# Performance work log

Measured on AMD Instinct MI355X. Metric: run time of the kernel, lower is better.

## Reference

```python
import jax, jax.numpy as jnp
import numpy as np

B, S, D, H = 2, 2048, 512, 8
DK = D // H


def setup_inputs() -> dict:
    key = jax.random.key(0)
    ks = jax.random.split(key, 7)
    scale = 1.0 / np.sqrt(D)
    return {
        "query": jax.random.normal(ks[0], (B, S, D), dtype=jnp.float32),
        "key": jax.random.normal(ks[1], (B, S, D), dtype=jnp.float32),
        "value": jax.random.normal(ks[2], (B, S, D), dtype=jnp.float32),
        "w_q": jax.random.normal(ks[3], (D, D), dtype=jnp.float32) * scale,
        "w_k": jax.random.normal(ks[4], (D, D), dtype=jnp.float32) * scale,
        "w_v": jax.random.normal(ks[5], (D, D), dtype=jnp.float32) * scale,
        "w_o": jax.random.normal(ks[6], (D, D), dtype=jnp.float32) * scale,
    }


def reference(query, key, value, w_q, w_k, w_v, w_o):
    # Linear projections (torch nn.Linear: x @ W.T), split into heads -> [b, h, s, dk]
    def proj(x, w):
        return (x @ w.T).reshape(B, -1, H, DK).transpose(0, 2, 1, 3)

    q = proj(query, w_q)
    k = proj(key, w_k)
    v = proj(value, w_v)

    # scaled dot-product attention (unfused, materializes [b,h,s,s] scores)
    scores = jnp.einsum("bhqd,bhkd->bhqk", q, k) / np.sqrt(DK)
    p_attn = jax.nn.softmax(scores, axis=-1)
    out = jnp.einsum("bhqk,bhkd->bhqd", p_attn, v)  # [b,h,s,dk]

    # merge heads and final projection
    out = out.transpose(0, 2, 1, 3).reshape(B, -1, D)
    out = out @ w_o.T
    return (out, p_attn)
```

## Files before the change

### kernel.cpp

```cpp
#include <hip/hip_runtime.h>
#include <hip/hip_bf16.h>
#include <cstdint>
#include <cstddef>

#define BB 2
#define SS 2048
#define DD 512
#define HH 8
#define DKK 64

typedef __attribute__((ext_vector_type(8))) short bf16x8;
typedef __attribute__((ext_vector_type(4))) float f32x4;

__device__ __forceinline__ unsigned short f2bf(float f) {
    union { float f; unsigned u; } v; v.f = f;
    unsigned u = v.u;
    return (unsigned short)((u + 0x7fffu + ((u >> 16) & 1u)) >> 16);
}
__device__ __forceinline__ unsigned pack2(float a, float b) {
    return (unsigned)f2bf(a) | ((unsigned)f2bf(b) << 16);
}

typedef const __attribute__((address_space(1))) unsigned int* gp_t;
typedef __attribute__((address_space(3))) unsigned int* lp_t;
__device__ __forceinline__ void gload_lds16(const void* g, void* l) {
    __builtin_amdgcn_global_load_lds((gp_t)g, (lp_t)l, 16, 0, 0);
}

#define VM_WAIT4 asm volatile("s_waitcnt vmcnt(4)" ::: "memory")
#define VM_WAIT0 asm volatile("s_waitcnt vmcnt(0)" ::: "memory")

template <bool ABF>
__device__ __forceinline__ void gemm64_core2(
    const void* __restrict__ Av, const float* __restrict__ W,
    unsigned short* smem, int bm, int bn, int tid, f32x4 acc[4])
{
    const int w = tid >> 6, lane = tid & 63, quad = lane >> 4, l15 = lane & 15;

    float4 ra[2][2], rw[2][2];
    auto loadRegs = [&](int k0) {
        if (!ABF) {
            const float* A = (const float*)Av;
            #pragma unroll
            for (int r = 0; r < 2; ++r) {
                int flat = r * 256 + tid;
                int row = flat >> 3, c = flat & 7, cs = c ^ (row & 7);
                const float* p = A + (size_t)(bm * 64 + row) * DD + k0 + cs * 8;
                ra[r][0] = *(const float4*)p;
                ra[r][1] = *(const float4*)(p + 4);
            }
        }
        #pragma unroll
        for (int r = 0; r < 2; ++r) {
            int flat = r * 256 + tid;
            int row = flat >> 3, c = flat & 7, cs = c ^ (row & 7);
            const float* p = W + (size_t)(bn * 64 + row) * DD + k0 + cs * 8;
            rw[r][0] = *(const float4*)p;
            rw[r][1] = *(const float4*)(p + 4);
        }
    };
    auto writeLDS = [&]() {
        #pragma unroll
        for (int r = 0; r < 2; ++r) {
            int flat = r * 256 + tid;
            if (!ABF)
                *(uint4*)&smem[flat * 8] = make_uint4(
                    pack2(ra[r][0].x, ra[r][0].y), pack2(ra[r][0].z, ra[r][0].w),
                    pack2(ra[r][1].x, ra[r][1].y), pack2(ra[r][1].z, ra[r][1].w));
            *(uint4*)&smem[4096 + flat * 8] = make_uint4(
                pack2(rw[r][0].x, rw[r][0].y), pack2(rw[r][0].z, rw[r][0].w),
                pack2(rw[r][1].x, rw[r][1].y), pack2(rw[r][1].z, rw[r][1].w));
        }
    };

    loadRegs(0);
    for (int k0 = 0; k0 < DD; k0 += 64) {
        if (ABF) {
            const unsigned short* A = (const unsigned short*)Av;
            #pragma unroll
            for (int r = 0; r < 2; ++r) {
                int flat = r * 256 + tid;
                int row = flat >> 3, c = flat & 7, cs = c ^ (row & 7);
                gload_lds16(A + (size_t)(bm * 64 + row) * DD + k0 + cs * 8, &smem[flat * 8]);
            }
        }
        writeLDS();
        __syncthreads();
        if (k0 + 64 < DD) loadRegs(k0 + 64);
        int mrow = w * 16 + l15;
        bf16x8 a0 = *(const bf16x8*)&smem[(mrow * 8 + (quad ^ (mrow & 7))) * 8];
        bf16x8 a1 = *(const bf16x8*)&smem[(mrow * 8 + ((quad + 4) ^ (mrow & 7))) * 8];
        #pragma unroll
        for (int nt = 0; nt < 4; ++nt) {
            int nrow = nt * 16 + l15;
            bf16x8 b0 = *(const bf16x8*)&smem[4096 + (nrow * 8 + (quad ^ (nrow & 7))) * 8];
            bf16x8 b1 = *(const bf16x8*)&smem[4096 + (nrow * 8 + ((quad + 4) ^ (nrow & 7))) * 8];
            acc[nt] = __builtin_amdgcn_mfma_f32_16x16x32_bf16(a0, b0, acc[nt], 0, 0, 0);
            acc[nt] = __builtin_amdgcn_mfma_f32_16x16x32_bf16(a1, b1, acc[nt], 0, 0, 0);
        }
        __syncthreads();
    }
}

__global__ __launch_bounds__(256) void k_gemm_qkv(
    const float* __restrict__ xq, const float* __restrict__ xk, const float* __restrict__ xv,
    const float* __restrict__ wq, const float* __restrict__ wk, const float* __restrict__ wv,
    unsigned short* __restrict__ Qw, unsigned short* __restrict__ Kw,
    unsigned short* __restrict__ Vt)
{
    __shared__ unsigned short smem[8192];
    const int z = blockIdx.z;
    const float* A = (z == 0) ? xq : (z == 1) ? xk : xv;
    const float* W = (z == 0) ? wq : (z == 1) ? wk : wv;
    const int bm = blockIdx.x, bn = blockIdx.y;
    const int tid = threadIdx.x, w = tid >> 6, lane = tid & 63, quad = lane >> 4, l15 = lane & 15;

    f32x4 acc[4];
    #pragma unroll
    for (int i = 0; i < 4; ++i) acc[i] = (f32x4){0.f, 0.f, 0.f, 0.f};
    gemm64_core2<false>(A, W, smem, bm, bn, tid, acc);

    if (z != 2) {
        const float sc = (z == 0) ? 0.125f : 1.0f;
        unsigned short* dbf = (z == 0) ? Qw : Kw;
        #pragma unroll
        for (int nt = 0; nt < 4; ++nt) {
            int n = bn * 64 + nt * 16 + l15;
            int h = n >> 6, dk = n & 63;
            #pragma unroll
            for (int rg = 0; rg < 4; ++rg) {
                int m = bm * 64 + w * 16 + quad * 4 + rg;
                int b = m >> 11, s = m & (SS - 1);
                dbf[(((size_t)(b * HH + h) * SS + s) << 6) + dk] = f2bf(acc[nt][rg] * sc);
            }
        }
    } else {
        unsigned short* T = smem;
        #pragma unroll
        for (int nt = 0; nt < 4; ++nt)
            #pragma unroll
            for (int rg = 0; rg < 4; ++rg)
                T[(w * 16 + quad * 4 + rg) * 72 + nt * 16 + l15] = f2bf(acc[nt][rg]);
        __syncthreads();
        int n = tid >> 2, s0 = (tid & 3) * 16;
        int ng = bn * 64 + n, h = ng >> 6, dk = ng & 63;
        int mg = bm * 64 + s0, b = mg >> 11, s = mg & (SS - 1);
        unsigned vals[8];
        #pragma unroll
        for (int i = 0; i < 8; ++i)
            vals[i] = (unsigned)T[(s0 + 2*i) * 72 + n] | ((unsigned)T[(s0 + 2*i + 1) * 72 + n] << 16);
        unsigned short* dp = Vt + ((size_t)(b * HH + h) * DKK + dk) * SS + s;
        ((uint4*)dp)[0] = make_uint4(vals[0], vals[1], vals[2], vals[3]);
        ((uint4*)dp)[1] = make_uint4(vals[4], vals[5], vals[6], vals[7]);
    }
}

__global__ __launch_bounds__(256) void k_attn(
    const unsigned short* __restrict__ Qw, const unsigned short* __restrict__ Kw,
    const unsigned short* __restrict__ Vt, unsigned short* __restrict__ AO,
    float* __restrict__ Linv)
{
    __shared__ unsigned short Kl[2][4096];
    __shared__ unsigned short Vl[2][4096];
    __shared__ unsigned short Pl[2][4][16][68];

    const int id = blockIdx.x;
    const int xcd = id & 7, j = id >> 3;
    const int bh = xcd * 2 + (j >> 5), qt = j & 31;

    const int tid = threadIdx.x, w = tid >> 6, lane = tid & 63, quad = lane >> 4, l15 = lane & 15;

    const unsigned short* Qb = Qw + ((size_t)bh * SS + qt * 64 + w * 16) * DKK;
    const unsigned short* Kb = Kw + (size_t)bh * SS * DKK;
    const unsigned short* Vb = Vt + (size_t)bh * DKK * SS;

    bf16x8 qa0 = *(const bf16x8*)&Qb[l15 * DKK + quad * 8];
    bf16x8 qa1 = *(const bf16x8*)&Qb[l15 * DKK + 32 + quad * 8];

    f32x4 oacc[4];
    #pragma unroll
    for (int i = 0; i < 4; ++i) oacc[i] = (f32x4){0.f, 0.f, 0.f, 0.f};
    float lsum[4] = {0.f, 0.f, 0.f, 0.f};

    auto stage = [&](int kt, int b) {
        #pragma unroll
        for (int r = 0; r < 2; ++r) {
            int flat = r * 256 + tid;
            int row = flat >> 3, c = flat & 7, cs = c ^ (row & 7);
            gload_lds16(Kb + (size_t)(kt * 64 + row) * DKK + cs * 8, &Kl[b][flat * 8]);
        }
        #pragma unroll
        for (int r = 0; r < 2; ++r) {
            int flat = r * 256 + tid;
            int row = flat >> 3, c = flat & 7, cs = c ^ (row & 7);
            gload_lds16(Vb + (size_t)row * SS + kt * 64 + cs * 8, &Vl[b][flat * 8]);
        }
    };

    stage(0, 0);
    stage(1, 1);

    const int NT = SS / 64;
    for (int kt = 0; kt < NT; ++kt) {
        if (kt < NT - 1) { VM_WAIT4; } else { VM_WAIT0; }
        __builtin_amdgcn_s_barrier();
        __builtin_amdgcn_sched_barrier(0);
        const int b = kt & 1;

        f32x4 sa[4];
        #pragma unroll
        for (int i = 0; i < 4; ++i) sa[i] = (f32x4){0.f, 0.f, 0.f, 0.f};
        __builtin_amdgcn_s_setprio(1);
        #pragma unroll
        for (int jt = 0; jt < 4; ++jt) {
            int row = jt * 16 + l15;
            bf16x8 b0 = *(const bf16x8*)&Kl[b][(row * 8 + (quad ^ (row & 7))) * 8];
            bf16x8 b1 = *(const bf16x8*)&Kl[b][(row * 8 + ((quad + 4) ^ (row & 7))) * 8];
            sa[jt] = __builtin_amdgcn_mfma_f32_16x16x32_bf16(qa0, b0, sa[jt], 0, 0, 0);
            sa[jt] = __builtin_amdgcn_mfma_f32_16x16x32_bf16(qa1, b1, sa[jt], 0, 0, 0);
        }
        __builtin_amdgcn_s_setprio(0);

        float ev[4][4];
        #pragma unroll
        for (int jt = 0; jt < 4; ++jt)
            #pragma unroll
            for (int rg = 0; rg < 4; ++rg)
                ev[jt][rg] = __expf(sa[jt][rg]);
        #pragma unroll
        for (int rg = 0; rg < 4; ++rg) {
            float s = ev[0][rg] + ev[1][rg] + ev[2][rg] + ev[3][rg];
            s += __shfl_xor(s, 1);
            s += __shfl_xor(s, 2);
            s += __shfl_xor(s, 4);
            s += __shfl_xor(s, 8);
            lsum[rg] += s;
        }
        #pragma unroll
        for (int jt = 0; jt < 4; ++jt)
            #pragma unroll
            for (int rg = 0; rg < 4; ++rg)
                Pl[b][w][quad * 4 + rg][jt * 16 + l15] = f2bf(ev[jt][rg]);
        bf16x8 pa0 = *(const bf16x8*)&Pl[b][w][l15][quad * 8];
        bf16x8 pa1 = *(const bf16x8*)&Pl[b][w][l15][32 + quad * 8];

        __builtin_amdgcn_s_setprio(1);
        #pragma unroll
        for (int dt = 0; dt < 4; ++dt) {
            int row = dt * 16 + l15;
            bf16x8 v0 = *(const bf16x8*)&Vl[b][(row * 8 + (quad ^ (row & 7))) * 8];
            bf16x8 v1 = *(const bf16x8*)&Vl[b][(row * 8 + ((quad + 4) ^ (row & 7))) * 8];
            oacc[dt] = __builtin_amdgcn_mfma_f32_16x16x32_bf16(pa0, v0, oacc[dt], 0, 0, 0);
            oacc[dt] = __builtin_amdgcn_mfma_f32_16x16x32_bf16(pa1, v1, oacc[dt], 0, 0, 0);
        }
        __builtin_amdgcn_s_setprio(0);

        __builtin_amdgcn_s_barrier();
        if (kt + 2 < NT) stage(kt + 2, b);
    }

    float linv[4];
    #pragma unroll
    for (int rg = 0; rg < 4; ++rg) linv[rg] = 1.0f / lsum[rg];

    const int b2 = bh >> 3, h = bh & 7;
    const int srow = qt * 64 + w * 16 + quad * 4;
    #pragma unroll
    for (int dt = 0; dt < 4; ++dt)
        #pragma unroll
        for (int rg = 0; rg < 4; ++rg)
            AO[((size_t)(b2 * SS + srow + rg) << 9) + h * 64 + dt * 16 + l15] =
                f2bf(oacc[dt][rg] * linv[rg]);

    if (l15 == 0) {
        #pragma unroll
        for (int rg = 0; rg < 4; ++rg)
            Linv[(size_t)bh * SS + srow + rg] = linv[rg];
    }
}

__global__ __launch_bounds__(256) void k_pwrite(
    const unsigned short* __restrict__ Qw, const unsigned short* __restrict__ Kw,
    const float* __restrict__ Linv, float* __restrict__ P)
{
    __shared__ float Tl[4][16][68];
    const int id = blockIdx.x;
    const int xcd = id & 7, j = id >> 3;
    const int bh = xcd * 2 + (j >> 7);
    const int rem = j & 127, qt = rem >> 2, ks = rem & 3;
    const int tid = threadIdx.x, w = tid >> 6, lane = tid & 63, quad = lane >> 4, l15 = lane & 15;

    const unsigned short* Qb = Qw + ((size_t)bh * SS + qt * 64 + w * 16) * DKK;
    bf16x8 qa0 = *(const bf16x8*)&Qb[l15 * DKK + quad * 8];
    bf16x8 qa1 = *(const bf16x8*)&Qb[l15 * DKK + 32 + quad * 8];

    float linv[4];
    #pragma unroll
    for (int rg = 0; rg < 4; ++rg)
        linv[rg] = Linv[(size_t)bh * SS + qt * 64 + w * 16 + quad * 4 + rg];

    const unsigned short* Kb = Kw + (size_t)bh * SS * DKK + (size_t)ks * 512 * DKK;
    float* Pb = P + (((size_t)bh * SS + qt * 64 + w * 16) << 11) + ks * 512;

    for (int kt = 0; kt < 8; ++kt) {
        const unsigned short* Kt = Kb + (size_t)kt * 64 * DKK;
        #pragma unroll
        for (int jt = 0; jt < 4; ++jt) {
            bf16x8 b0 = *(const bf16x8*)&Kt[(jt * 16 + l15) * DKK + quad * 8];
            bf16x8 b1 = *(const bf16x8*)&Kt[(jt * 16 + l15) * DKK + 32 + quad * 8];
            f32x4 sa = (f32x4){0.f, 0.f, 0.f, 0.f};
            sa = __builtin_amdgcn_mfma_f32_16x16x32_bf16(qa0, b0, sa, 0, 0, 0);
            sa = __builtin_amdgcn_mfma_f32_16x16x32_bf16(qa1, b1, sa, 0, 0, 0);
            #pragma unroll
            for (int rg = 0; rg < 4; ++rg)
                Tl[w][quad * 4 + rg][jt * 16 + l15] = __expf(sa[rg]) * linv[rg];
        }
        #pragma unroll
        for (int c = 0; c < 4; ++c) {
            int row = c * 4 + quad;
            f32x4 val = *(const f32x4*)&Tl[w][row][l15 * 4];
            __builtin_nontemporal_store(val,
                (f32x4*)(Pb + ((size_t)row << 11) + kt * 64 + l15 * 4));
        }
    }
}

__global__ __launch_bounds__(256) void k_gemm_o(
    const unsigned short* __restrict__ A, const float* __restrict__ W,
    float* __restrict__ out)
{
    __shared__ unsigned short smem[8192];
    const int bm = blockIdx.x, bn = blockIdx.y;
    const int tid = threadIdx.x, w = tid >> 6, lane = tid & 63, quad = lane >> 4, l15 = lane & 15;
    f32x4 acc[4];
    #pragma unroll
    for (int i = 0; i < 4; ++i) acc[i] = (f32x4){0.f, 0.f, 0.f, 0.f};
    gemm64_core2<true>(A, W, smem, bm, bn, tid, acc);
    #pragma unroll
    for (int nt = 0; nt < 4; ++nt)
        #pragma unroll
        for (int rg = 0; rg < 4; ++rg)
            out[(size_t)(bm * 64 + w * 16 + quad * 4 + rg) * DD + bn * 64 + nt * 16 + l15] =
                acc[nt][rg];
}

extern "C" void kernel_launch(void* const* d_in, const int* in_sizes, int n_in,
                              void* d_out, int out_size, void* d_ws, size_t ws_size,
                              hipStream_t stream) {
    const float* q  = (const float*)d_in[0];
    const float* k  = (const float*)d_in[1];
    const float* v  = (const float*)d_in[2];
    const float* wq = (const float*)d_in[3];
    const float* wk = (const float*)d_in[4];
    const float* wv = (const float*)d_in[5];
    const float* wo = (const float*)d_in[6];

    float* out = (float*)d_out;
    float* P   = out + (size_t)BB * SS * DD;

    const size_t NX = (size_t)BB * SS * DD;

    unsigned short* Qw   = (unsigned short*)d_ws;
    unsigned short* Kw   = Qw + NX;
    unsigned short* Vt   = Kw + NX;
    unsigned short* AO   = Vt + NX;
    float*          Linv = (float*)(AO + NX);

    k_gemm_qkv<<<dim3(64, 8, 3), 256, 0, stream>>>(q, k, v, wq, wk, wv, Qw, Kw, Vt);
    k_attn<<<dim3(512), 256, 0, stream>>>(Qw, Kw, Vt, AO, Linv);
    k_pwrite<<<dim3(2048), 256, 0, stream>>>(Qw, Kw, Linv, P);
    k_gemm_o<<<dim3(64, 8), 256, 0, stream>>>(AO, wo, out);
}
```

Before: 400.0 us.

## Split attention KV loop across two blocks and merge partial outputs

The attention kernel now splits the key sequence in half, so 1024 blocks each process 16 key tiles instead of 512 blocks processing 32. This gives more parallelism on a GPU with many CUs. Unnormalized fp32 partial outputs and row sums go to scratch space carved out of the P output buffer, and a new merge kernel combines them, normalizes, writes bf16 AO, and writes Linv. This relies on no running-max subtraction, as in the previous code, and adds an extra kernel launch plus fp32 partial traffic. The scratch reuse is safe because k_pwrite overwrites P afterwards.

```diff
diff --git a/kernel.cpp b/kernel.cpp
--- a/kernel.cpp
+++ b/kernel.cpp
@@ -157,8 +157,8 @@
 
 __global__ __launch_bounds__(256) void k_attn(
     const unsigned short* __restrict__ Qw, const unsigned short* __restrict__ Kw,
-    const unsigned short* __restrict__ Vt, unsigned short* __restrict__ AO,
-    float* __restrict__ Linv)
+    const unsigned short* __restrict__ Vt, float* __restrict__ Opart,
+    float* __restrict__ Lpart)
 {
     __shared__ unsigned short Kl[2][4096];
     __shared__ unsigned short Vl[2][4096];
@@ -166,7 +166,8 @@
 
     const int id = blockIdx.x;
     const int xcd = id & 7, j = id >> 3;
-    const int bh = xcd * 2 + (j >> 5), qt = j & 31;
+    const int bh = xcd * 2 + (j >> 6);
+    const int rem = j & 63, qt = rem >> 1, ks = rem & 1;
 
     const int tid = threadIdx.x, w = tid >> 6, lane = tid & 63, quad = lane >> 4, l15 = lane & 15;
 
@@ -197,19 +198,20 @@
         }
     };
 
-    stage(0, 0);
-    stage(1, 1);
-
-    const int NT = SS / 64;
-    for (int kt = 0; kt < NT; ++kt) {
-        if (kt < NT - 1) { VM_WAIT4; } else { VM_WAIT0; }
+    const int NT = 16;
+    const int base = ks * NT;
+    stage(base + 0, 0);
+    stage(base + 1, 1);
+
+    for (int i = 0; i < NT; ++i) {
+        if (i < NT - 1) { VM_WAIT4; } else { VM_WAIT0; }
         __builtin_amdgcn_s_barrier();
         __builtin_amdgcn_sched_barrier(0);
-        const int b = kt & 1;
+        const int b = i & 1;
 
         f32x4 sa[4];
         #pragma unroll
-        for (int i = 0; i < 4; ++i) sa[i] = (f32x4){0.f, 0.f, 0.f, 0.f};
+        for (int ii = 0; ii < 4; ++ii) sa[ii] = (f32x4){0.f, 0.f, 0.f, 0.f};
         __builtin_amdgcn_s_setprio(1);
         #pragma unroll
         for (int jt = 0; jt < 4; ++jt) {
@@ -256,27 +258,57 @@
         __builtin_amdgcn_s_setprio(0);
 
         __builtin_amdgcn_s_barrier();
-        if (kt + 2 < NT) stage(kt + 2, b);
-    }
-
-    float linv[4];
-    #pragma unroll
-    for (int rg = 0; rg < 4; ++rg) linv[rg] = 1.0f / lsum[rg];
-
+        if (i + 2 < NT) stage(base + i + 2, b);
+    }
+
+    const int srow = qt * 64 + w * 16 + quad * 4;
+    float* Ob = Opart + (((size_t)(bh * 2 + ks) * SS + srow) << 6);
+    #pragma unroll
+    for (int dt = 0; dt < 4; ++dt)
+        #pragma unroll
+        for (int rg = 0; rg < 4; ++rg)
+            Ob[((size_t)rg << 6) + dt * 16 + l15] = oacc[dt][rg];
+
+    if (l15 == 0) {
+        #pragma unroll
+        for (int rg = 0; rg < 4; ++rg)
+            Lpart[(size_t)(bh * 2 + ks) * SS + srow + rg] = lsum[rg];
+    }
+}
+
+__global__ __launch_bounds__(256) void k_merge(
+    const float* __restrict__ Opart, const float* __restrict__ Lpart,
+    unsigned short* __restrict__ AO, float* __restrict__ Linv)
+{
+    const int qt = blockIdx.x, bh = blockIdx.y;
+    const int tid = threadIdx.x;
+    const int r = tid >> 2, c0 = (tid & 3) * 16;
+    const int s = qt * 64 + r;
+
+    const float l0 = Lpart[(size_t)(bh * 2 + 0) * SS + s];
+    const float l1 = Lpart[(size_t)(bh * 2 + 1) * SS + s];
+    const float linv = 1.0f / (l0 + l1);
+
+    const float* p0 = Opart + ((((size_t)(bh * 2 + 0) * SS + s) << 6) + c0);
+    const float* p1 = Opart + ((((size_t)(bh * 2 + 1) * SS + s) << 6) + c0);
+    float o[16];
+    #pragma unroll
+    for (int i = 0; i < 4; ++i) {
+        float4 a = ((const float4*)p0)[i];
+        float4 b = ((const float4*)p1)[i];
+        o[i*4+0] = (a.x + b.x) * linv;
+        o[i*4+1] = (a.y + b.y) * linv;
+        o[i*4+2] = (a.z + b.z) * linv;
+        o[i*4+3] = (a.w + b.w) * linv;
+    }
     const int b2 = bh >> 3, h = bh & 7;
-    const int srow = qt * 64 + w * 16 + quad * 4;
-    #pragma unroll
-    for (int dt = 0; dt < 4; ++dt)
-        #pragma unroll
-        for (int rg = 0; rg < 4; ++rg)
-            AO[((size_t)(b2 * SS + srow + rg) << 9) + h * 64 + dt * 16 + l15] =
-                f2bf(oacc[dt][rg] * linv[rg]);
-
-    if (l15 == 0) {
-        #pragma unroll
-        for (int rg = 0; rg < 4; ++rg)
-            Linv[(size_t)bh * SS + srow + rg] = linv[rg];
-    }
+    unsigned short* dp = AO + (((size_t)(b2 * SS + s)) << 9) + h * 64 + c0;
+    ((uint4*)dp)[0] = make_uint4(pack2(o[0],o[1]), pack2(o[2],o[3]),
+                                 pack2(o[4],o[5]), pack2(o[6],o[7]));
+    ((uint4*)dp)[1] = make_uint4(pack2(o[8],o[9]), pack2(o[10],o[11]),
+                                 pack2(o[12],o[13]), pack2(o[14],o[15]));
+
+    if ((tid & 3) == 0) Linv[(size_t)bh * SS + s] = linv;
 }
 
 __global__ __launch_bounds__(256) void k_pwrite(
@@ -360,6 +392,9 @@
 
     const size_t NX = (size_t)BB * SS * DD;
 
+    float* Opart = P;
+    float* Lpart = Opart + (size_t)32 * SS * DKK;
+
     unsigned short* Qw   = (unsigned short*)d_ws;
     unsigned short* Kw   = Qw + NX;
     unsigned short* Vt   = Kw + NX;
@@ -367,7 +402,8 @@
     float*          Linv = (float*)(AO + NX);
 
     k_gemm_qkv<<<dim3(64, 8, 3), 256, 0, stream>>>(q, k, v, wq, wk, wv, Qw, Kw, Vt);
-    k_attn<<<dim3(512), 256, 0, stream>>>(Qw, Kw, Vt, AO, Linv);
+    k_attn<<<dim3(1024), 256, 0, stream>>>(Qw, Kw, Vt, Opart, Lpart);
+    k_merge<<<dim3(32, 16), 256, 0, stream>>>(Opart, Lpart, AO, Linv);
     k_pwrite<<<dim3(2048), 256, 0, stream>>>(Qw, Kw, Linv, P);
     k_gemm_o<<<dim3(64, 8), 256, 0, stream>>>(AO, wo, out);
 }
```

Result: no change. 405.1 us (+1.3%).
